# Performance work log

Hardware: AMD Instinct MI355X
Metric: run time of the kernel (lower is better)

The kernel has to match this reference:

```python
import jax, jax.numpy as jnp
import numpy as np

N_, C_, H_, W_ = 8, 256, 64, 64
HEADS = 8
KS = 3
K2 = KS * KS
OUT = 256
HD = OUT // HEADS
STRIDE = 1
PAD = 1


def setup_inputs() -> dict:
    key = jax.random.key(0)
    ks = jax.random.split(key, 8)
    s = 0.05
    return {
        "input_features": jax.random.normal(ks[0], (N_, C_, H_, W_), jnp.float32),
        "Wq": jax.random.normal(ks[1], (OUT, C_), jnp.float32) * s,
        "Wk": jax.random.normal(ks[2], (OUT, C_), jnp.float32) * s,
        "Wv": jax.random.normal(ks[3], (OUT, C_), jnp.float32) * s,
        "off_w": jax.random.normal(ks[4], (HEADS * K2 * 2, C_, KS, KS), jnp.float32) * 0.01,
        "off_b": jnp.zeros((HEADS * K2 * 2,), jnp.float32),
        "attn_w": jax.random.normal(ks[5], (HEADS * K2, C_, KS, KS), jnp.float32) * 0.01,
        "attn_b": jnp.zeros((HEADS * K2,), jnp.float32),
        "Wo": jax.random.normal(ks[6], (OUT, OUT), jnp.float32) * s,
    }


def _conv2d(x, w, b):
    out = jax.lax.conv_general_dilated(
        x, w, (STRIDE, STRIDE), [(PAD, PAD), (PAD, PAD)],
        dimension_numbers=("NCHW", "OIHW", "NCHW"))
    return out + b[None, :, None, None]


def reference(input_features, Wq, Wk, Wv, off_w, off_b, attn_w, attn_b, Wo):
    x = input_features
    N, C, H, W = x.shape
    # query/key are projected but never used downstream in the original module
    q = jnp.einsum("oc,nchw->nohw", Wq, x)
    k = jnp.einsum("oc,nchw->nohw", Wk, x)
    v = jnp.einsum("oc,nchw->nohw", Wv, x)  # [N, OUT, H, W]

    offsets = _conv2d(x, off_w, off_b)                       # [N, HEADS*K2*2, Ho, Wo]
    aw = jax.nn.sigmoid(_conv2d(x, attn_w, attn_b))          # [N, HEADS*K2, Ho, Wo]
    Ho, Wo_sp = offsets.shape[2], offsets.shape[3]

    gx_base = jnp.linspace(-1.0, 1.0, Wo_sp)
    gy_base = jnp.linspace(-1.0, 1.0, Ho)

    # per-head, per-point (x,y) offsets, scaled by 2/[W,H] as in the source
    off = offsets.reshape(N, HEADS, K2, 2, Ho, Wo_sp)
    gx = gx_base[None, None, None, None, :] + off[:, :, :, 0] * (2.0 / W)  # [N,H,K2,Ho,Wo]
    gy = gy_base[None, None, None, :, None] + off[:, :, :, 1] * (2.0 / H)

    # grid_sample bilinear, align_corners=True, padding_mode='zeros'
    xp = (gx + 1.0) * 0.5 * (W - 1)
    yp = (gy + 1.0) * 0.5 * (H - 1)
    x0 = jnp.floor(xp).astype(jnp.int32)
    y0 = jnp.floor(yp).astype(jnp.int32)
    x1 = x0 + 1
    y1 = y0 + 1
    wx1 = xp - x0
    wx0 = 1.0 - wx1
    wy1 = yp - y0
    wy0 = 1.0 - wy1

    vf = v.reshape(N, HEADS, HD, H * W)

    def corner(yi, xi, wgt):
        valid = ((yi >= 0) & (yi < H) & (xi >= 0) & (xi < W)).astype(v.dtype)
        idx = (jnp.clip(yi, 0, H - 1) * W + jnp.clip(xi, 0, W - 1)).reshape(N, HEADS, -1)
        g = jnp.take_along_axis(vf, idx[:, :, None, :], axis=3)
        g = g.reshape(N, HEADS, HD, K2, Ho, Wo_sp)
        return g * (wgt * valid)[:, :, None]

    sampled = (corner(y0, x0, wy0 * wx0) + corner(y0, x1, wy0 * wx1)
               + corner(y1, x0, wy1 * wx0) + corner(y1, x1, wy1 * wx1))

    awr = aw.reshape(N, HEADS, K2, Ho, Wo_sp)
    head_out = jnp.einsum("nhckxy,nhkxy->nhcxy", sampled, awr)  # weighted sum over K2 points
    combined = head_out.reshape(N, OUT, Ho, Wo_sp)
    return jnp.einsum("oc,nchw->nohw", Wo, combined)
```

## Files before the change

kernel.cpp:

```cpp
#include <hip/hip_runtime.h>
#include <math.h>

#define N_    8
#define C_    256
#define H_    64
#define W_    64
#define HW    4096
#define OUT_  256
#define HEADS 8
#define HD    32
#define K2    9
#define OFFCH 144
#define AWCH  72
#define KTOT  2304
#define WPROWS 256
#define ABASE 16896

typedef __bf16 bf16x8 __attribute__((ext_vector_type(8)));
typedef __bf16 bf16x4 __attribute__((ext_vector_type(4)));
typedef float  f32x4  __attribute__((ext_vector_type(4)));

__device__ __forceinline__ void gload_lds16(const void* g, void* l) {
  __builtin_amdgcn_global_load_lds(
      (const __attribute__((address_space(1))) void*)g,
      (__attribute__((address_space(3))) void*)l, 16, 0, 0);
}

__device__ __forceinline__ void conv_body(
    __bf16* smem, const __bf16* __restrict__ xp, const __bf16* __restrict__ Wp,
    const float* __restrict__ biasp, const __bf16* __restrict__ zbuf,
    __bf16* __restrict__ P2, int yt, int bn, int n, int tid)
{
  const int y0 = yt << 1;
  const int lw = tid & 63, wv = tid >> 6;
  const int lr = lw & 15, lg = lw >> 4;

  f32x4 acc[8][2];
#pragma unroll
  for (int m = 0; m < 8; ++m)
#pragma unroll
    for (int nt = 0; nt < 2; ++nt) acc[m][nt] = (f32x4){0.f, 0.f, 0.f, 0.f};

  if (tid < 64) {
    int p = tid & 3, cs = (tid >> 2) & 1, r = (tid >> 3) & 3, buf = tid >> 5;
    int col = cs ? 65 : 0;
    *(uint4*)&smem[((buf * 4 + r) * 66 + col) * 32 + p * 8] =
        make_uint4(0u, 0u, 0u, 0u);
  }

  int aoff[3][4];
#pragma unroll
  for (int d = 0; d < 3; ++d)
#pragma unroll
    for (int mm = 0; mm < 4; ++mm) {
      int col = (mm << 4) + lr + d;
      int p = lg ^ ((col >> 1) & 3);
      aoff[d][mm] = col * 32 + p * 8;
    }
  int boff[2];
#pragma unroll
  for (int nt = 0; nt < 2; ++nt) {
    int col = (nt << 4) + lr;
    int p = lg ^ ((col >> 1) & 3);
    boff[nt] = ABASE + wv * 3072 + col * 32 + p * 8;
  }

  const int scg = lw & 3;
  const __bf16* gB[2];
#pragma unroll
  for (int jj = 0; jj < 2; ++jj) {
    int col = (jj << 4) + (lw >> 2);
    int cg = scg ^ ((col >> 1) & 3);
    gB[jj] = Wp + (size_t)(bn * 128 + wv * 32 + col) * KTOT + (cg << 3);
  }
  const __bf16* gA[4];
  int aAdd;
  {
    int y = y0 - 1 + wv;
    bool valid = ((unsigned)y < (unsigned)H_);
    aAdd = valid ? 1 : 0;
#pragma unroll
    for (int k = 0; k < 4; ++k) {
      int col = 1 + (k << 4) + (lw >> 2);
      int cg = scg ^ ((col >> 1) & 3);
      gA[k] = valid
          ? xp + ((size_t)(n * HW) + y * W_ + (col - 1)) * C_ + (cg << 3)
          : zbuf;
    }
  }

  auto stageB = [&](int elemOff, int pbuf) {
#pragma unroll
    for (int jj = 0; jj < 2; ++jj)
      gload_lds16(gB[jj] + elemOff,
                  &smem[ABASE + wv * 3072 + pbuf * 1024 + (jj << 9)]);
  };
  auto stageA = [&](int c0elem, int buf) {
    const int add = aAdd ? c0elem : 0;
#pragma unroll
    for (int k = 0; k < 4; ++k)
      gload_lds16(gA[k] + add,
                  &smem[((buf * 4 + wv) * 66 + 1 + (k << 4)) * 32]);
  };

  stageA(0, 0);
  stageB(0 * C_ + 0, 0);
  stageB(3 * C_ + 0, 1);
  asm volatile("s_waitcnt vmcnt(4)" ::: "memory");
  __builtin_amdgcn_s_barrier();
  asm volatile("" ::: "memory");

  for (int cc = 0; cc < 4; ++cc) {
    const bool lastcc = (cc == 3);
#pragma unroll
    for (int sub = 0; sub < 2; ++sub) {
      const int ci = (cc << 1) + sub;
      const int abuf = sub;
      bf16x8 a[8];
#pragma unroll
      for (int s = 0; s < 9; ++s) {
        const int dxp = s / 3, dy = s % 3;
        const int pbR = s % 3;
        const int pbW = (s + 2) % 3;
        const bool lastSlice = lastcc && (sub == 1);

        if (s == 1 && ci < 7) stageA((ci + 1) << 5, sub ^ 1);

        if (!(lastSlice && s >= 7)) {
          const int sn  = (s + 2 < 9) ? (s + 2) : (s - 7);
          const int cin = (s + 2 < 9) ? ci : (ci + 1);
          const int tn  = (sn % 3) * 3 + (sn / 3);
          stageB(tn * C_ + (cin << 5), pbW);
        }

        if (lastSlice && s == 8)
          asm volatile("s_waitcnt vmcnt(0)" ::: "memory");
        else if (lastSlice && s == 7)
          asm volatile("s_waitcnt vmcnt(2)" ::: "memory");
        else if ((s == 1 || s == 2) && ci < 7)
          asm volatile("s_waitcnt vmcnt(8)" ::: "memory");
        else
          asm volatile("s_waitcnt vmcnt(4)" ::: "memory");

        if (dy == 0) {
#pragma unroll
          for (int m = 0; m < 8; ++m) {
            const int rr = (m >> 2);
            a[m] = *(const bf16x8*)&smem[aoff[dxp][m & 3] +
                                         (abuf * 4 + rr) * 2112];
          }
        } else {
#pragma unroll
          for (int m = 0; m < 4; ++m) a[m] = a[m + 4];
#pragma unroll
          for (int m = 4; m < 8; ++m) {
            const int rr = 1 + dy;
            a[m] = *(const bf16x8*)&smem[aoff[dxp][m & 3] +
                                         (abuf * 4 + rr) * 2112];
          }
        }
        bf16x8 b[2];
#pragma unroll
        for (int nt = 0; nt < 2; ++nt)
          b[nt] = *(const bf16x8*)&smem[boff[nt] + (pbR << 10)];

        __builtin_amdgcn_s_setprio(1);
#pragma unroll
        for (int m = 0; m < 8; ++m)
#pragma unroll
          for (int nt = 0; nt < 2; ++nt)
            acc[m][nt] = __builtin_amdgcn_mfma_f32_16x16x32_bf16(
                a[m], b[nt], acc[m][nt], 0, 0, 0);
        __builtin_amdgcn_s_setprio(0);

        if (s == 8 && !lastSlice) {
          __builtin_amdgcn_s_barrier();
          asm volatile("" ::: "memory");
        }
      }
    }
  }

#pragma unroll
  for (int nt = 0; nt < 2; ++nt) {
    const int co = bn * 128 + wv * 32 + (nt << 4) + lr;
    if (co < 216) {
      const float bias = biasp[co];
      int idx;
      if (co < OFFCH) {
        int hh = co / 18;
        idx = (hh << 5) + (co - 18 * hh);
      } else {
        int r = co - OFFCH;
        int hh = r / 9;
        idx = (hh << 5) + 18 + (r - 9 * hh);
      }
#pragma unroll
      for (int m = 0; m < 8; ++m) {
#pragma unroll
        for (int reg = 0; reg < 4; ++reg) {
          const int sl = (m << 4) + (lg << 2) + reg;
          const int yout = y0 + (sl >> 6), xo = sl & 63;
          float v = acc[m][nt][reg] + bias;
          if (co >= OFFCH) v = 1.f / (1.f + expf(-v));
          P2[((size_t)n * HW + yout * W_ + xo) * 256 + idx] = (__bf16)v;
        }
      }
    }
  }
}

template <int MODE>
__device__ __forceinline__ void gemm_body(
    __bf16* smem, const __bf16* __restrict__ A, const __bf16* __restrict__ Wb,
    __bf16* __restrict__ out_b, float* __restrict__ out_f,
    int st, int bn, int n, int tid)
{
  const int s0 = st << 7;
  const int lw = tid & 63, wv = tid >> 6;
  const int lr = lw & 15, lg = lw >> 4;
  const int sm_base = wv << 5;

  f32x4 acc[2][8];
#pragma unroll
  for (int m = 0; m < 2; ++m)
#pragma unroll
    for (int nt = 0; nt < 8; ++nt) acc[m][nt] = (f32x4){0.f, 0.f, 0.f, 0.f};

  int aoff[2];
#pragma unroll
  for (int m = 0; m < 2; ++m) {
    int row = sm_base + (m << 4) + lr;
    int p = lg ^ ((row >> 1) & 3);
    aoff[m] = row * 32 + p * 8;
  }
  int boff[8];
#pragma unroll
  for (int nt = 0; nt < 8; ++nt) {
    int row = (nt << 4) + lr;
    int p = lg ^ ((row >> 1) & 3);
    boff[nt] = 12288 + row * 32 + p * 8;
  }

  const __bf16* gA[2];
  const __bf16* gB[2];
#pragma unroll
  for (int jj = 0; jj < 2; ++jj) {
    int j = wv * 2 + jj;
    int row = (j << 4) + (lw >> 2);
    int cg = (lw & 3) ^ ((row >> 1) & 3);
    gA[jj] = A + ((size_t)n * HW + s0 + row) * 256 + (cg << 3);
    gB[jj] = Wb + ((size_t)((bn << 7) + row)) * 256 + (cg << 3);
  }

  auto stage = [&](int k, int buf) {
    const int koff = k << 5;
#pragma unroll
    for (int jj = 0; jj < 2; ++jj)
      gload_lds16(gA[jj] + koff, &smem[buf * 4096 + ((wv * 2 + jj) << 9)]);
#pragma unroll
    for (int jj = 0; jj < 2; ++jj)
      gload_lds16(gB[jj] + koff,
                  &smem[12288 + buf * 4096 + ((wv * 2 + jj) << 9)]);
  };

  stage(0, 0);
  stage(1, 1);

#pragma unroll
  for (int k = 0; k < 8; ++k) {
    if (k < 7)
      asm volatile("s_waitcnt vmcnt(4)" ::: "memory");
    else
      asm volatile("s_waitcnt vmcnt(0)" ::: "memory");
    __builtin_amdgcn_s_barrier();
    asm volatile("" ::: "memory");

    if (k + 2 < 8) stage(k + 2, (k + 2) % 3);

    const int buf = k % 3;
    bf16x8 a[2], b[8];
#pragma unroll
    for (int m = 0; m < 2; ++m)
      a[m] = *(const bf16x8*)&smem[aoff[m] + buf * 4096];
#pragma unroll
    for (int nt = 0; nt < 8; ++nt)
      b[nt] = *(const bf16x8*)&smem[boff[nt] + buf * 4096];

    __builtin_amdgcn_s_setprio(1);
#pragma unroll
    for (int m = 0; m < 2; ++m)
#pragma unroll
      for (int nt = 0; nt < 8; ++nt)
        acc[m][nt] = __builtin_amdgcn_mfma_f32_16x16x32_bf16(
            a[m], b[nt], acc[m][nt], 0, 0, 0);
    __builtin_amdgcn_s_setprio(0);
  }

#pragma unroll
  for (int m = 0; m < 2; ++m) {
#pragma unroll
    for (int nt = 0; nt < 8; ++nt) {
      const int co = (bn << 7) + (nt << 4) + lr;
      if (MODE == 0) {
#pragma unroll
        for (int reg = 0; reg < 4; ++reg) {
          const int sm = sm_base + (m << 4) + (lg << 2) + reg;
          out_b[((size_t)n * HW + s0 + sm) * 256 + co] = (__bf16)acc[m][nt][reg];
        }
      } else {
        const int sm = sm_base + (m << 4) + (lg << 2);
        float4 v4 = make_float4(acc[m][nt][0], acc[m][nt][1],
                                acc[m][nt][2], acc[m][nt][3]);
        *(float4*)&out_f[((size_t)(n * 256 + co)) * HW + s0 + sm] = v4;
      }
    }
  }
}

__global__ __launch_bounds__(256) void fused_pre_kernel(
    const float* __restrict__ x, __bf16* __restrict__ xp,
    const float* __restrict__ off_w, const float* __restrict__ off_b,
    const float* __restrict__ attn_w, const float* __restrict__ attn_b,
    const float* __restrict__ Wv, const float* __restrict__ Wo,
    __bf16* __restrict__ Wp, float* __restrict__ biasp,
    __bf16* __restrict__ zbuf, __bf16* __restrict__ Wvb,
    __bf16* __restrict__ Wob)
{
  const int b = blockIdx.x;
  const int tid = threadIdx.x;
  __shared__ float tile[64][65];

  if (b < 2048) {
    const int c0 = (b & 3) << 6;
    const int y  = (b >> 2) & 63;
    const int n  = b >> 8;
    const int tx = tid & 63, tg = tid >> 6;
#pragma unroll
    for (int i = 0; i < 16; ++i) {
      int cl = tg + (i << 2);
      tile[cl][tx] = x[((size_t)(n * C_ + c0 + cl) * H_ + y) * W_ + tx];
    }
    __syncthreads();
#pragma unroll
    for (int i = 0; i < 16; ++i) {
      int xl = tg + (i << 2);
      xp[((size_t)(n * HW) + y * W_ + xl) * C_ + c0 + tx] = (__bf16)tile[tx][xl];
    }
  } else {
    const int bb = b - 2048;
    const int c = tid;
    if (bb < 256) {
      const int co = bb;
      if (co == 0) {
        *(uint4*)&zbuf[(size_t)c * 8] = make_uint4(0u, 0u, 0u, 0u);
      }
      const float* base = nullptr;
      if (co < OFFCH)      base = off_w  + ((size_t)co * C_ + c) * 9;
      else if (co < 216)   base = attn_w + ((size_t)(co - OFFCH) * C_ + c) * 9;
#pragma unroll
      for (int t = 0; t < 9; ++t) {
        float w = base ? base[t] : 0.f;
        Wp[(size_t)co * KTOT + t * C_ + c] = (__bf16)w;
      }
      if (c == 0) {
        float bv = 0.f;
        if (co < OFFCH) bv = off_b[co];
        else if (co < 216) bv = attn_b[co - OFFCH];
        biasp[co] = bv;
      }
    } else if (bb < 512) {
      const int i = (bb - 256) * 256 + c;
      Wvb[i] = (__bf16)Wv[i];
    } else {
      const int i = (bb - 512) * 256 + c;
      Wob[i] = (__bf16)Wo[i];
    }
  }
}

__global__ __launch_bounds__(256) void fused_cv_kernel(
    const __bf16* __restrict__ xp, const __bf16* __restrict__ Wp,
    const float* __restrict__ biasp, const __bf16* __restrict__ zbuf,
    __bf16* __restrict__ P2, const __bf16* __restrict__ Wvb,
    __bf16* __restrict__ vtb)
{
  __shared__ __align__(16) __bf16 smem[16896 + 12288];
  const int bn = blockIdx.y;
  if (bn < 2)
    conv_body(smem, xp, Wp, biasp, zbuf, P2, blockIdx.x, bn, blockIdx.z,
              threadIdx.x);
  else
    gemm_body<0>(smem, xp, Wvb, vtb, nullptr, blockIdx.x, bn - 2, blockIdx.z,
                 threadIdx.x);
}

__global__ __launch_bounds__(256) void wo_kernel(
    const __bf16* __restrict__ comb, const __bf16* __restrict__ Wob,
    float* __restrict__ out)
{
  __shared__ __align__(16) __bf16 smem[24576];
  gemm_body<1>(smem, comb, Wob, nullptr, out, blockIdx.x, blockIdx.y,
               blockIdx.z, threadIdx.x);
}

__global__ __launch_bounds__(256) void sample_kernel(
    const __bf16* __restrict__ vtb, const __bf16* __restrict__ P2,
    __bf16* __restrict__ comb)
{
  const int b  = blockIdx.x;
  const int yp = b & 31;
  const int h  = (b >> 5) & 7;
  const int n  = b >> 8;
  const int yb = yp << 1;
  const int tid = threadIdx.x;
  const int cg  = tid & 1;
  const int pt  = tid >> 1;
  const int yloc = pt >> 6, xq = pt & 63;
  const int y = yb + yloc;
  const int wv = tid >> 6;

  __shared__ __align__(16) __bf16 vsl[9 * 64 * 32];

  const int xs = tid >> 2, cs = tid & 3;
  const __bf16* vsrc =
      vtb + ((size_t)n * HW) * 256 + (h << 5) + (cs << 3) + (size_t)xs * 256;
#pragma unroll
  for (int r = 0; r < 9; ++r) {
    int yy = yb - 3 + r;
    if ((unsigned)yy < (unsigned)H_)
      gload_lds16(vsrc + (size_t)yy * (64 * 256),
                  &vsl[(r * 64 + (wv << 4)) * 32]);
  }

  const __bf16* prow = P2 + ((size_t)n * HW + y * 64 + xq) * 256 + (h << 5);
  bf16x8 p0 = *(const bf16x8*)(prow);
  bf16x8 p1 = *(const bf16x8*)(prow + 8);
  bf16x8 p2 = *(const bf16x8*)(prow + 16);
  bf16x4 p3 = *(const bf16x4*)(prow + 24);

  __syncthreads();

  float acc[16];
#pragma unroll
  for (int j = 0; j < 16; ++j) acc[j] = 0.f;

  const __bf16* vbase = vtb + ((size_t)n * HW) * 256 + (h << 5) + (cg << 4);

#pragma unroll
  for (int k = 0; k < K2; ++k) {
    float offx, offy, a;
    if (k < 4)      { offx = (float)p0[2 * k];       offy = (float)p0[2 * k + 1]; }
    else if (k < 8) { offx = (float)p1[2 * (k - 4)]; offy = (float)p1[2 * (k - 4) + 1]; }
    else            { offx = (float)p2[0];           offy = (float)p2[1]; }
    if (k < 6)      a = (float)p2[2 + k];
    else            a = (float)p3[k - 6];

    const float xpf = (float)xq + offx * (63.f / 64.f);
    const float ypf = (float)y  + offy * (63.f / 64.f);
    const float fx0 = floorf(xpf), fy0 = floorf(ypf);
    const int ix0 = (int)fx0, iy0 = (int)fy0;
    const float wx1 = xpf - fx0, wx0 = 1.f - wx1;
    const float wy1 = ypf - fy0, wy0 = 1.f - wy1;

#pragma unroll
    for (int cy = 0; cy < 2; ++cy) {
      const int yi = iy0 + cy;
      if ((unsigned)yi >= (unsigned)H_) continue;
      const float wy = cy ? wy1 : wy0;
      const int ridx = yi - (yb - 3);
#pragma unroll
      for (int cx = 0; cx < 2; ++cx) {
        const int xi = ix0 + cx;
        if ((unsigned)xi >= (unsigned)W_) continue;
        const float cw = a * wy * (cx ? wx1 : wx0);
        bf16x8 v0, v1;
        if ((unsigned)ridx < 9u) {
          const __bf16* lp = &vsl[(ridx * 64 + xi) * 32 + (cg << 4)];
          v0 = *(const bf16x8*)lp;
          v1 = *(const bf16x8*)(lp + 8);
        } else {
          const __bf16* gp = vbase + (size_t)(yi * W_ + xi) * 256;
          v0 = *(const bf16x8*)gp;
          v1 = *(const bf16x8*)(gp + 8);
        }
#pragma unroll
        for (int j = 0; j < 8; ++j) acc[j] = fmaf(cw, (float)v0[j], acc[j]);
#pragma unroll
        for (int j = 0; j < 8; ++j)
          acc[8 + j] = fmaf(cw, (float)v1[j], acc[8 + j]);
      }
    }
  }

  bf16x8 r0, r1;
#pragma unroll
  for (int j = 0; j < 8; ++j) { r0[j] = (__bf16)acc[j]; r1[j] = (__bf16)acc[8 + j]; }
  __bf16* crow = comb + ((size_t)n * HW + y * 64 + xq) * 256 + (h << 5) + (cg << 4);
  *(bf16x8*)crow = r0;
  *(bf16x8*)(crow + 8) = r1;
}

extern "C" void kernel_launch(void* const* d_in, const int* in_sizes, int n_in,
                              void* d_out, int out_size, void* d_ws,
                              size_t ws_size, hipStream_t stream)
{
  const float* x      = (const float*)d_in[0];
  const float* Wv     = (const float*)d_in[3];
  const float* off_w  = (const float*)d_in[4];
  const float* off_b  = (const float*)d_in[5];
  const float* attn_w = (const float*)d_in[6];
  const float* attn_b = (const float*)d_in[7];
  const float* Wo     = (const float*)d_in[8];
  float* out = (float*)d_out;

  __bf16* vtb   = (__bf16*)d_ws;
  __bf16* xp    = vtb + (size_t)N_ * HW * OUT_;
  __bf16* comb  = xp + (size_t)N_ * HW * C_;
  __bf16* P2    = comb + (size_t)N_ * HW * OUT_;
  __bf16* Wp    = P2 + (size_t)N_ * HW * 256;
  __bf16* Wvb   = Wp + (size_t)WPROWS * KTOT;
  __bf16* Wob   = Wvb + (size_t)OUT_ * C_;
  __bf16* zbuf  = Wob + (size_t)OUT_ * OUT_;
  float*  biasp = (float*)(zbuf + 2048);

  fused_pre_kernel<<<dim3(2816), 256, 0, stream>>>(
      x, xp, off_w, off_b, attn_w, attn_b, Wv, Wo, Wp, biasp, zbuf, Wvb, Wob);
  fused_cv_kernel<<<dim3(32, 4, N_), 256, 0, stream>>>(xp, Wp, biasp, zbuf, P2,
                                                       Wvb, vtb);
  sample_kernel<<<dim3(N_ * HEADS * 32), 256, 0, stream>>>(vtb, P2, comb);
  wo_kernel<<<dim3(32, 2, N_), 256, 0, stream>>>(comb, Wob, out);
}
```

Before: 106.9 us.

## Give each sample thread all 32 head channels and four output rows per block

The sampling kernel now assigns one output pixel per thread, covering all 32 head channels instead of splitting them across two threads. Each block handles four rows instead of two and stages 11 value rows in LDS instead of 9, which halves the grid. This cuts redundant offset and weight math and the halo reload overhead per output row. The cost is twice the accumulator registers per thread, which may lower occupancy, and fewer blocks to spread across the GPU.

```diff
diff --git a/kernel.cpp b/kernel.cpp
--- a/kernel.cpp
+++ b/kernel.cpp
@@ -409,24 +409,22 @@
     __bf16* __restrict__ comb)
 {
   const int b  = blockIdx.x;
-  const int yp = b & 31;
-  const int h  = (b >> 5) & 7;
-  const int n  = b >> 8;
-  const int yb = yp << 1;
+  const int y4 = b & 15;
+  const int h  = (b >> 4) & 7;
+  const int n  = b >> 7;
+  const int yb = y4 << 2;
   const int tid = threadIdx.x;
-  const int cg  = tid & 1;
-  const int pt  = tid >> 1;
-  const int yloc = pt >> 6, xq = pt & 63;
+  const int yloc = tid >> 6, xq = tid & 63;
   const int y = yb + yloc;
   const int wv = tid >> 6;
 
-  __shared__ __align__(16) __bf16 vsl[9 * 64 * 32];
+  __shared__ __align__(16) __bf16 vsl[11 * 64 * 32];
 
   const int xs = tid >> 2, cs = tid & 3;
   const __bf16* vsrc =
       vtb + ((size_t)n * HW) * 256 + (h << 5) + (cs << 3) + (size_t)xs * 256;
 #pragma unroll
-  for (int r = 0; r < 9; ++r) {
+  for (int r = 0; r < 11; ++r) {
     int yy = yb - 3 + r;
     if ((unsigned)yy < (unsigned)H_)
       gload_lds16(vsrc + (size_t)yy * (64 * 256),
@@ -441,11 +439,11 @@
 
   __syncthreads();
 
-  float acc[16];
-#pragma unroll
-  for (int j = 0; j < 16; ++j) acc[j] = 0.f;
-
-  const __bf16* vbase = vtb + ((size_t)n * HW) * 256 + (h << 5) + (cg << 4);
+  float acc[32];
+#pragma unroll
+  for (int j = 0; j < 32; ++j) acc[j] = 0.f;
+
+  const __bf16* vbase = vtb + ((size_t)n * HW) * 256 + (h << 5);
 
 #pragma unroll
   for (int k = 0; k < K2; ++k) {
@@ -474,31 +472,44 @@
         const int xi = ix0 + cx;
         if ((unsigned)xi >= (unsigned)W_) continue;
         const float cw = a * wy * (cx ? wx1 : wx0);
-        bf16x8 v0, v1;
-        if ((unsigned)ridx < 9u) {
-          const __bf16* lp = &vsl[(ridx * 64 + xi) * 32 + (cg << 4)];
+        bf16x8 v0, v1, v2, v3;
+        if ((unsigned)ridx < 11u) {
+          const __bf16* lp = &vsl[(ridx * 64 + xi) * 32];
           v0 = *(const bf16x8*)lp;
           v1 = *(const bf16x8*)(lp + 8);
+          v2 = *(const bf16x8*)(lp + 16);
+          v3 = *(const bf16x8*)(lp + 24);
         } else {
           const __bf16* gp = vbase + (size_t)(yi * W_ + xi) * 256;
           v0 = *(const bf16x8*)gp;
           v1 = *(const bf16x8*)(gp + 8);
-        }
-#pragma unroll
-        for (int j = 0; j < 8; ++j) acc[j] = fmaf(cw, (float)v0[j], acc[j]);
-#pragma unroll
-        for (int j = 0; j < 8; ++j)
-          acc[8 + j] = fmaf(cw, (float)v1[j], acc[8 + j]);
-      }
-    }
-  }
-
-  bf16x8 r0, r1;
-#pragma unroll
-  for (int j = 0; j < 8; ++j) { r0[j] = (__bf16)acc[j]; r1[j] = (__bf16)acc[8 + j]; }
-  __bf16* crow = comb + ((size_t)n * HW + y * 64 + xq) * 256 + (h << 5) + (cg << 4);
+          v2 = *(const bf16x8*)(gp + 16);
+          v3 = *(const bf16x8*)(gp + 24);
+        }
+#pragma unroll
+        for (int j = 0; j < 8; ++j) {
+          acc[j]      = fmaf(cw, (float)v0[j], acc[j]);
+          acc[8 + j]  = fmaf(cw, (float)v1[j], acc[8 + j]);
+          acc[16 + j] = fmaf(cw, (float)v2[j], acc[16 + j]);
+          acc[24 + j] = fmaf(cw, (float)v3[j], acc[24 + j]);
+        }
+      }
+    }
+  }
+
+  bf16x8 r0, r1, r2, r3;
+#pragma unroll
+  for (int j = 0; j < 8; ++j) {
+    r0[j] = (__bf16)acc[j];
+    r1[j] = (__bf16)acc[8 + j];
+    r2[j] = (__bf16)acc[16 + j];
+    r3[j] = (__bf16)acc[24 + j];
+  }
+  __bf16* crow = comb + ((size_t)n * HW + y * 64 + xq) * 256 + (h << 5);
   *(bf16x8*)crow = r0;
   *(bf16x8*)(crow + 8) = r1;
+  *(bf16x8*)(crow + 16) = r2;
+  *(bf16x8*)(crow + 24) = r3;
 }
 
 extern "C" void kernel_launch(void* const* d_in, const int* in_sizes, int n_in,
@@ -528,6 +539,6 @@
       x, xp, off_w, off_b, attn_w, attn_b, Wv, Wo, Wp, biasp, zbuf, Wvb, Wob);
   fused_cv_kernel<<<dim3(32, 4, N_), 256, 0, stream>>>(xp, Wp, biasp, zbuf, P2,
                                                        Wvb, vtb);
-  sample_kernel<<<dim3(N_ * HEADS * 32), 256, 0, stream>>>(vtb, P2, comb);
+  sample_kernel<<<dim3(N_ * HEADS * 16), 256, 0, stream>>>(vtb, P2, comb);
   wo_kernel<<<dim3(32, 2, N_), 256, 0, stream>>>(comb, Wob, out);
 }
```

After: 110.9 us. 3.8% more time.
